# Optimization experiments

Measured on AMD Instinct MI355X. Metric: run time of the kernel, lower is better.

Reference implementation:

```python
import jax, jax.numpy as jnp
import numpy as np

SIZE = 128
B, S = 32, 8192


def setup_inputs() -> dict:
    key = jax.random.key(0)
    kx, = jax.random.split(key, 1)
    x = jax.random.normal(kx, (B, S, SIZE), dtype=jnp.float32)
    return {
        "x": x,
        # DyT params
        "alpha": jnp.ones((1,), jnp.float32) * 0.5,
        "dyt_weight": jnp.ones((SIZE,), jnp.float32),
        "dyt_bias": jnp.zeros((SIZE,), jnp.float32),
        # FourierForwardNetwork params
        "a_real": jnp.ones((SIZE,), jnp.float32),
        "a_imag": jnp.zeros((SIZE,), jnp.float32),
        "b_real": jnp.ones((SIZE,), jnp.float32),
        "b_imag": jnp.zeros((SIZE,), jnp.float32),
        "ffn_bias": jnp.zeros((SIZE,), jnp.float32),
    }


def reference(x, alpha, dyt_weight, dyt_bias, a_real, a_imag, b_real, b_imag, ffn_bias):
    # DyT: tanh(alpha * x) * weight + bias
    h = jnp.tanh(alpha * x) * dyt_weight + dyt_bias  # [B, S, SIZE]
    # FourierForwardNetwork. NOTE: in the original torch code the first
    # spectral branch (multiply by a, ifft, +bias, gelu) is DEAD CODE --
    # its result is overwritten by `X = torch.fft.fft(x + 0j)`. The actual
    # output is ifft(fft(h) * b).real, reproduced faithfully here.
    b = b_real + 1j * b_imag  # [SIZE] complex
    X = jnp.fft.fft(h.astype(jnp.complex64), axis=-1)  # [B, S, SIZE] complex64
    y = jnp.fft.ifft(X * b, axis=-1).real.astype(x.dtype)
    # Residual connection of FourierFFNBlock
    return y + x
```

## Files before the change

### kernel.cpp

```cpp
#include <hip/hip_runtime.h>

#define SIZE 128
#define PAD 136

typedef short short8 __attribute__((ext_vector_type(8)));
typedef float f32x4 __attribute__((ext_vector_type(4)));

__device__ __forceinline__ unsigned short f2bf(float f) {
    unsigned int u = __float_as_uint(f);
    unsigned int r = u + 0x7FFFu + ((u >> 16) & 1u);
    return (unsigned short)(r >> 16);
}
__device__ __forceinline__ float bf2f(unsigned short h) {
    return __uint_as_float(((unsigned int)h) << 16);
}

__global__ void build_gt(const float* __restrict__ br, const float* __restrict__ bi,
                         const float* __restrict__ w, const float* __restrict__ bias,
                         unsigned short* __restrict__ Gt, float* __restrict__ C0) {
    __shared__ float gr[SIZE];
    const int t = threadIdx.x;
    float acc = 0.0f;
    for (int j = 0; j < SIZE; ++j) {
        int p = (j * t) & 127;
        float a = (float)p * (1.0f / 64.0f);
        acc += br[j] * cospif(a) - bi[j] * sinpif(a);
    }
    gr[t] = acc * (1.0f / 128.0f);
    __syncthreads();
    float c0 = 0.0f;
    for (int k = 0; k < SIZE; ++k) {
        const float g = gr[(t - k) & 127];
        c0 += bias[k] * g;
        Gt[t * SIZE + k] = f2bf(w[k] * g);
    }
    C0[t] = c0;
}

__global__ __launch_bounds__(256, 4) void fourier_main(
    const float* __restrict__ x, const float* __restrict__ alpha_p,
    const unsigned short* __restrict__ Gt, const float* __restrict__ C0,
    float* __restrict__ out) {
    __shared__ unsigned short hA[64 * PAD];
    __shared__ unsigned short oA[64 * PAD];

    const int tid = threadIdx.x;
    const int lane = tid & 63;
    const int wid = tid >> 6;
    const int lrow = lane & 15;
    const int slot = lane >> 4;
    const int colb = wid * 32;

    const float a2 = 2.0f * alpha_p[0];
    const unsigned base = (unsigned)blockIdx.x * (64u * SIZE);

    const int rl = tid >> 5;
    const int cl = (tid & 31) * 4;

    float4 xr[8];
#pragma unroll
    for (int j = 0; j < 8; ++j)
        xr[j] = *reinterpret_cast<const float4*>(&x[base + j * 1024 + tid * 4]);

#pragma unroll
    for (int j = 0; j < 8; ++j) {
        ushort4 hq;
        float e, r;
        e = __expf(a2 * xr[j].x); r = __builtin_amdgcn_rcpf(1.0f + e);
        hq.x = f2bf(fmaf(-2.0f, r, 1.0f));
        e = __expf(a2 * xr[j].y); r = __builtin_amdgcn_rcpf(1.0f + e);
        hq.y = f2bf(fmaf(-2.0f, r, 1.0f));
        e = __expf(a2 * xr[j].z); r = __builtin_amdgcn_rcpf(1.0f + e);
        hq.z = f2bf(fmaf(-2.0f, r, 1.0f));
        e = __expf(a2 * xr[j].w); r = __builtin_amdgcn_rcpf(1.0f + e);
        hq.w = f2bf(fmaf(-2.0f, r, 1.0f));
        *reinterpret_cast<ushort4*>(&hA[(j * 8 + rl) * PAD + cl]) = hq;
    }

    short8 gf[2][4];
    float4 c0v[2];
#pragma unroll
    for (int nt = 0; nt < 2; ++nt) {
        const int c = colb + nt * 16 + lrow;
#pragma unroll
        for (int kt = 0; kt < 4; ++kt)
            gf[nt][kt] = *reinterpret_cast<const short8*>(
                &Gt[c * SIZE + kt * 32 + slot * 8]);
        c0v[nt] = *reinterpret_cast<const float4*>(&C0[colb + nt * 16 + slot * 4]);
    }

    __syncthreads();

#pragma unroll
    for (int mt = 0; mt < 4; ++mt) {
        short8 hf[4];
#pragma unroll
        for (int kt = 0; kt < 4; ++kt)
            hf[kt] = *reinterpret_cast<const short8*>(
                &hA[(mt * 16 + lrow) * PAD + kt * 32 + slot * 8]);
#pragma unroll
        for (int nt = 0; nt < 2; ++nt) {
            f32x4 a = {0.f, 0.f, 0.f, 0.f};
#pragma unroll
            for (int kt = 0; kt < 4; ++kt)
                a = __builtin_amdgcn_mfma_f32_16x16x32_bf16(gf[nt][kt], hf[kt], a,
                                                            0, 0, 0);
            ushort4 o;
            o.x = f2bf(a[0] + c0v[nt].x);
            o.y = f2bf(a[1] + c0v[nt].y);
            o.z = f2bf(a[2] + c0v[nt].z);
            o.w = f2bf(a[3] + c0v[nt].w);
            *reinterpret_cast<ushort4*>(
                &oA[(mt * 16 + lrow) * PAD + colb + nt * 16 + slot * 4]) = o;
        }
    }

    __syncthreads();

#pragma unroll
    for (int j = 0; j < 8; ++j) {
        const ushort4 ov =
            *reinterpret_cast<const ushort4*>(&oA[(j * 8 + rl) * PAD + cl]);
        float4 r;
        r.x = bf2f(ov.x) + xr[j].x;
        r.y = bf2f(ov.y) + xr[j].y;
        r.z = bf2f(ov.z) + xr[j].z;
        r.w = bf2f(ov.w) + xr[j].w;
        *reinterpret_cast<float4*>(&out[base + j * 1024 + tid * 4]) = r;
    }
}

extern "C" void kernel_launch(void* const* d_in, const int* in_sizes, int n_in,
                              void* d_out, int out_size, void* d_ws, size_t ws_size,
                              hipStream_t stream) {
    const float* x = (const float*)d_in[0];
    const float* alpha = (const float*)d_in[1];
    const float* dyt_w = (const float*)d_in[2];
    const float* dyt_b = (const float*)d_in[3];
    const float* b_real = (const float*)d_in[6];
    const float* b_imag = (const float*)d_in[7];
    float* out = (float*)d_out;

    unsigned short* Gt = (unsigned short*)d_ws;
    float* C0 = (float*)((char*)d_ws + SIZE * SIZE * 2);

    build_gt<<<1, 128, 0, stream>>>(b_real, b_imag, dyt_w, dyt_b, Gt, C0);

    const int rows = out_size / SIZE;
    const int nblocks = rows / 64;
    fourier_main<<<nblocks, 256, 0, stream>>>(x, alpha, Gt, C0, out);
}
```

Baseline: 71.01 us.

## Make blocks persistent over row tiles with double-buffered LDS prefetch and direct output stores

Each block now walks 8 tiles of 32 rows. It prefetches the next tile's x into registers while running MFMA on the current tile, and double-buffers the bf16 tanh activations in LDS. The output staging buffer is gone: the residual is added by re-reading x in the MFMA fragment layout, and results go straight to global memory with fp32 precision. This is meant to hide load latency and amortise the Gt fragment loads. In exchange x is read twice (the second read may hit cache), output stores are less coalesced, and the grid has fewer blocks.

```diff
diff --git a/kernel.cpp b/kernel.cpp
--- a/kernel.cpp
+++ b/kernel.cpp
@@ -1,7 +1,9 @@
 #include <hip/hip_runtime.h>
 
 #define SIZE 128
-#define PAD 136
+#define ROWS 32
+#define TPB 8
+#define PITCH 136
 
 typedef short short8 __attribute__((ext_vector_type(8)));
 typedef float f32x4 __attribute__((ext_vector_type(4)));
@@ -10,9 +12,6 @@
     unsigned int u = __float_as_uint(f);
     unsigned int r = u + 0x7FFFu + ((u >> 16) & 1u);
     return (unsigned short)(r >> 16);
-}
-__device__ __forceinline__ float bf2f(unsigned short h) {
-    return __uint_as_float(((unsigned int)h) << 16);
 }
 
 __global__ void build_gt(const float* __restrict__ br, const float* __restrict__ bi,
@@ -41,41 +40,16 @@
     const float* __restrict__ x, const float* __restrict__ alpha_p,
     const unsigned short* __restrict__ Gt, const float* __restrict__ C0,
     float* __restrict__ out) {
-    __shared__ unsigned short hA[64 * PAD];
-    __shared__ unsigned short oA[64 * PAD];
+    __shared__ unsigned short hA[2][ROWS * PITCH];
 
     const int tid = threadIdx.x;
     const int lane = tid & 63;
-    const int wid = tid >> 6;
+    const int wv = tid >> 6;
     const int lrow = lane & 15;
     const int slot = lane >> 4;
-    const int colb = wid * 32;
+    const int colb = wv * 32;
 
-    const float a2 = 2.0f * alpha_p[0];
-    const unsigned base = (unsigned)blockIdx.x * (64u * SIZE);
-
-    const int rl = tid >> 5;
-    const int cl = (tid & 31) * 4;
-
-    float4 xr[8];
-#pragma unroll
-    for (int j = 0; j < 8; ++j)
-        xr[j] = *reinterpret_cast<const float4*>(&x[base + j * 1024 + tid * 4]);
-
-#pragma unroll
-    for (int j = 0; j < 8; ++j) {
-        ushort4 hq;
-        float e, r;
-        e = __expf(a2 * xr[j].x); r = __builtin_amdgcn_rcpf(1.0f + e);
-        hq.x = f2bf(fmaf(-2.0f, r, 1.0f));
-        e = __expf(a2 * xr[j].y); r = __builtin_amdgcn_rcpf(1.0f + e);
-        hq.y = f2bf(fmaf(-2.0f, r, 1.0f));
-        e = __expf(a2 * xr[j].z); r = __builtin_amdgcn_rcpf(1.0f + e);
-        hq.z = f2bf(fmaf(-2.0f, r, 1.0f));
-        e = __expf(a2 * xr[j].w); r = __builtin_amdgcn_rcpf(1.0f + e);
-        hq.w = f2bf(fmaf(-2.0f, r, 1.0f));
-        *reinterpret_cast<ushort4*>(&hA[(j * 8 + rl) * PAD + cl]) = hq;
-    }
+    const float a2l = 2.0f * 1.44269504f * alpha_p[0];
 
     short8 gf[2][4];
     float4 c0v[2];
@@ -89,44 +63,76 @@
         c0v[nt] = *reinterpret_cast<const float4*>(&C0[colb + nt * 16 + slot * 4]);
     }
 
-    __syncthreads();
+    const unsigned blockBase = (unsigned)blockIdx.x * (TPB * ROWS * SIZE);
+    const int srow = tid >> 5;
+    const int scol = (tid & 31) * 4;
+
+    auto stage = [&](int t, float4 (&xn)[4]) __attribute__((always_inline)) {
+        const float* src = x + blockBase + (unsigned)t * (ROWS * SIZE);
+#pragma unroll
+        for (int i = 0; i < 4; ++i)
+            xn[i] = *reinterpret_cast<const float4*>(&src[i * 1024 + tid * 4]);
+    };
+    auto hwrite = [&](int buf, const float4 (&xn)[4]) __attribute__((always_inline)) {
+#pragma unroll
+        for (int i = 0; i < 4; ++i) {
+            ushort4 hq;
+            float e;
+            e = __builtin_amdgcn_exp2f(a2l * xn[i].x);
+            hq.x = f2bf(fmaf(-2.0f, __builtin_amdgcn_rcpf(1.0f + e), 1.0f));
+            e = __builtin_amdgcn_exp2f(a2l * xn[i].y);
+            hq.y = f2bf(fmaf(-2.0f, __builtin_amdgcn_rcpf(1.0f + e), 1.0f));
+            e = __builtin_amdgcn_exp2f(a2l * xn[i].z);
+            hq.z = f2bf(fmaf(-2.0f, __builtin_amdgcn_rcpf(1.0f + e), 1.0f));
+            e = __builtin_amdgcn_exp2f(a2l * xn[i].w);
+            hq.w = f2bf(fmaf(-2.0f, __builtin_amdgcn_rcpf(1.0f + e), 1.0f));
+            *reinterpret_cast<ushort4*>(&hA[buf][(i * 8 + srow) * PITCH + scol]) = hq;
+        }
+    };
+    auto compute = [&](int t) __attribute__((always_inline)) {
+        const unsigned tb = blockBase + (unsigned)t * (ROWS * SIZE);
+        const unsigned short* hb = &hA[t & 1][0];
+#pragma unroll
+        for (int mt = 0; mt < 2; ++mt) {
+            const int r = mt * 16 + lrow;
+            short8 hf[4];
+#pragma unroll
+            for (int kt = 0; kt < 4; ++kt)
+                hf[kt] = *reinterpret_cast<const short8*>(
+                    &hb[r * PITCH + kt * 32 + slot * 8]);
+#pragma unroll
+            for (int nt = 0; nt < 2; ++nt) {
+                f32x4 a = {0.f, 0.f, 0.f, 0.f};
+#pragma unroll
+                for (int kt = 0; kt < 4; ++kt)
+                    a = __builtin_amdgcn_mfma_f32_16x16x32_bf16(gf[nt][kt], hf[kt],
+                                                                a, 0, 0, 0);
+                const unsigned off =
+                    tb + (unsigned)r * SIZE + (unsigned)(colb + nt * 16 + slot * 4);
+                const float4 xa = *reinterpret_cast<const float4*>(&x[off]);
+                float4 o;
+                o.x = a[0] + c0v[nt].x + xa.x;
+                o.y = a[1] + c0v[nt].y + xa.y;
+                o.z = a[2] + c0v[nt].z + xa.z;
+                o.w = a[3] + c0v[nt].w + xa.w;
+                *reinterpret_cast<float4*>(&out[off]) = o;
+            }
+        }
+    };
+
+    float4 xn[4];
+    stage(0, xn);
+    hwrite(0, xn);
+    asm volatile("s_waitcnt lgkmcnt(0)\n\ts_barrier" ::: "memory");
 
 #pragma unroll
-    for (int mt = 0; mt < 4; ++mt) {
-        short8 hf[4];
-#pragma unroll
-        for (int kt = 0; kt < 4; ++kt)
-            hf[kt] = *reinterpret_cast<const short8*>(
-                &hA[(mt * 16 + lrow) * PAD + kt * 32 + slot * 8]);
-#pragma unroll
-        for (int nt = 0; nt < 2; ++nt) {
-            f32x4 a = {0.f, 0.f, 0.f, 0.f};
-#pragma unroll
-            for (int kt = 0; kt < 4; ++kt)
-                a = __builtin_amdgcn_mfma_f32_16x16x32_bf16(gf[nt][kt], hf[kt], a,
-                                                            0, 0, 0);
-            ushort4 o;
-            o.x = f2bf(a[0] + c0v[nt].x);
-            o.y = f2bf(a[1] + c0v[nt].y);
-            o.z = f2bf(a[2] + c0v[nt].z);
-            o.w = f2bf(a[3] + c0v[nt].w);
-            *reinterpret_cast<ushort4*>(
-                &oA[(mt * 16 + lrow) * PAD + colb + nt * 16 + slot * 4]) = o;
+    for (int t = 0; t < TPB; ++t) {
+        if (t + 1 < TPB) stage(t + 1, xn);
+        compute(t);
+        if (t + 1 < TPB) {
+            hwrite((t + 1) & 1, xn);
+            asm volatile("s_waitcnt lgkmcnt(0)\n\ts_barrier" ::: "memory");
         }
-    }
-
-    __syncthreads();
-
-#pragma unroll
-    for (int j = 0; j < 8; ++j) {
-        const ushort4 ov =
-            *reinterpret_cast<const ushort4*>(&oA[(j * 8 + rl) * PAD + cl]);
-        float4 r;
-        r.x = bf2f(ov.x) + xr[j].x;
-        r.y = bf2f(ov.y) + xr[j].y;
-        r.z = bf2f(ov.z) + xr[j].z;
-        r.w = bf2f(ov.w) + xr[j].w;
-        *reinterpret_cast<float4*>(&out[base + j * 1024 + tid * 4]) = r;
     }
 }
 
@@ -147,6 +153,6 @@
     build_gt<<<1, 128, 0, stream>>>(b_real, b_imag, dyt_w, dyt_b, Gt, C0);
 
     const int rows = out_size / SIZE;
-    const int nblocks = rows / 64;
+    const int nblocks = rows / (ROWS * TPB);
     fourier_main<<<nblocks, 256, 0, stream>>>(x, alpha, Gt, C0, out);
 }
```

New measurement: 76.88 us. 8.3% more time.
